# Optimization experiments

Hardware: AMD Instinct MI355X
Metric: run time of the kernel (lower is better)

Reference implementation:

```python
import jax, jax.numpy as jnp
import numpy as np

N_NODES = 100000
N_EDGES = 3200000
Q = 32
DT = 0.1
XI_MIN, XI_MAX = 0.0, 75.0


def setup_inputs() -> dict:
    key = jax.random.key(0)
    k1, k2, k3, k4, k5, k6 = jax.random.split(key, 6)
    f_distribution = jax.random.uniform(k1, (N_NODES, Q), dtype=jnp.float32)
    collision_term = jax.random.normal(k2, (N_NODES, Q), dtype=jnp.float32) * 0.01
    source_term = jax.random.normal(k3, (N_NODES, Q), dtype=jnp.float32) * 0.01
    edge_weight = jax.random.uniform(k4, (N_EDGES,), dtype=jnp.float32)
    src = jax.random.randint(k5, (N_EDGES,), 0, N_NODES, dtype=jnp.int32)
    dst = jax.random.randint(k6, (N_EDGES,), 0, N_NODES, dtype=jnp.int32)
    return {
        "f_distribution": f_distribution,
        "collision_term": collision_term,
        "source_term": source_term,
        "edge_weight": edge_weight,
        "src": src,
        "dst": dst,
    }


def _transport(f, edge_weight, src, dst):
    # xi velocity grid, one scalar per mesoscale channel q
    xi = jnp.linspace(XI_MIN, XI_MAX, Q, dtype=f.dtype)  # [Q]
    n = f.shape[0]
    # out-degree of each node in the (self-loop-free) graph
    out_deg = jax.ops.segment_sum(jnp.ones_like(edge_weight), src, num_segments=n)
    inv_out_deg = 1.0 / jnp.maximum(out_deg, 1.0)  # guard isolated nodes
    # per-edge message: (1/out_deg[src]) * xi * (f[dst]-f[src]) * w_e  -> [E, Q]
    f_diff = f[dst] - f[src]
    msg = (inv_out_deg[src] * edge_weight)[:, None] * xi[None, :] * f_diff
    # inflow: sum of messages at the destination node (original graph update_all)
    inflow = jax.ops.segment_sum(msg, dst, num_segments=n)
    # outflow: same per-edge quantity scattered back to the source node
    # (reverse-graph update_all with in_degree of reverse == out_degree of original)
    outflow = jax.ops.segment_sum(msg, src, num_segments=n)
    return outflow - inflow


def reference(f_distribution, collision_term, source_term, edge_weight, src, dst):
    f = jnp.maximum(f_distribution, 0.0)
    transport = _transport(f, edge_weight, src, dst)
    f_new = f - DT * (transport - collision_term - source_term)
    return jnp.maximum(f_new, 0.0)
```

## Files before the change

### kernel.cpp

```cpp
#include <hip/hip_runtime.h>
#include <hip/hip_fp16.h>

#define N_NODES 100000
#define N_EDGES 3200000
#define QCH 32
#define QP 16
#define DT_C 0.1f

#define NCHUNK 256
#define CHUNK_E (N_EDGES / NCHUNK)
#define HALF_NODES 50000
#define WORDS_HALF 12500
#define WORDS_TOT 25000

__global__ __launch_bounds__(256) void hist_kernel(const int* __restrict__ src,
                                                   unsigned int* __restrict__ part) {
    __shared__ unsigned int h[WORDS_HALF];
    int tid = threadIdx.x;
    int chunk = blockIdx.x >> 1;
    int rh = blockIdx.x & 1;
    int r0 = rh * HALF_NODES;
    for (int i = tid; i < WORDS_HALF; i += 256) h[i] = 0u;
    __syncthreads();
    int e0 = chunk * CHUNK_E;
    for (int e = e0 + tid; e < e0 + CHUNK_E; e += 256) {
        int n = src[e] - r0;
        if ((unsigned)n < HALF_NODES)
            atomicAdd(&h[n >> 2], 1u << (8 * (n & 3)));
    }
    __syncthreads();
    unsigned int* dstp = part + (size_t)chunk * WORDS_TOT + rh * WORDS_HALF;
    for (int i = tid; i < WORDS_HALF; i += 256) dstp[i] = h[i];
}

__global__ __launch_bounds__(256) void degsum_kernel(
        const unsigned int* __restrict__ part, float* __restrict__ deg) {
    int wd = blockIdx.x * 256 + threadIdx.x;
    if (wd >= WORDS_TOT) return;
    unsigned int s0 = 0, s1 = 0, s2 = 0, s3 = 0;
#pragma unroll 8
    for (int i = 0; i < NCHUNK; ++i) {
        unsigned int v = part[(size_t)i * WORDS_TOT + wd];
        s0 += v & 255u;
        s1 += (v >> 8) & 255u;
        s2 += (v >> 16) & 255u;
        s3 += v >> 24;
    }
    *(float4*)(deg + 4 * wd) =
        make_float4((float)s0, (float)s1, (float)s2, (float)s3);
}

__global__ void edge_kernel_h2(const float2* __restrict__ f2,
                               const float* __restrict__ w,
                               const int* __restrict__ src,
                               const int* __restrict__ dst,
                               const float* __restrict__ deg,
                               __half2* __restrict__ trans, int E) {
    long long t = (long long)blockIdx.x * blockDim.x + threadIdx.x;
    int e = (int)(t >> 4);
    int qp = (int)(t & 15);
    if (e >= E) return;
    int s = src[e];
    int d = dst[e];
    float coef = w[e] / fmaxf(deg[s], 1.0f);
    float2 fs = f2[s * QP + qp];
    float2 fd = f2[d * QP + qp];
    float xi0 = (75.0f / 31.0f) * (float)(2 * qp);
    float xi1 = (75.0f / 31.0f) * (float)(2 * qp + 1);
    float m0 = coef * xi0 * (fmaxf(fd.x, 0.0f) - fmaxf(fs.x, 0.0f));
    float m1 = coef * xi1 * (fmaxf(fd.y, 0.0f) - fmaxf(fs.y, 0.0f));
    unsafeAtomicAdd(&trans[s * QP + qp], __floats2half2_rn(m0, m1));
    unsafeAtomicAdd(&trans[d * QP + qp], __floats2half2_rn(-m0, -m1));
}

__global__ void final_f4(const float4* __restrict__ fdist,
                         const float4* __restrict__ coll,
                         const float4* __restrict__ srct,
                         const __half2* __restrict__ trans,
                         float4* __restrict__ out, int n4) {
    int i = blockIdx.x * blockDim.x + threadIdx.x;
    if (i >= n4) return;
    float2 t0 = __half22float2(trans[2 * i]);
    float2 t1 = __half22float2(trans[2 * i + 1]);
    float4 fr = fdist[i];
    float4 cl = coll[i];
    float4 st = srct[i];
    float4 o;
    o.x = fmaxf(fmaxf(fr.x, 0.0f) - DT_C * (t0.x - cl.x - st.x), 0.0f);
    o.y = fmaxf(fmaxf(fr.y, 0.0f) - DT_C * (t0.y - cl.y - st.y), 0.0f);
    o.z = fmaxf(fmaxf(fr.z, 0.0f) - DT_C * (t1.x - cl.z - st.z), 0.0f);
    o.w = fmaxf(fmaxf(fr.w, 0.0f) - DT_C * (t1.y - cl.w - st.w), 0.0f);
    out[i] = o;
}

__global__ void deg_kernel_f(const int* __restrict__ src,
                             float* __restrict__ deg, int E) {
    int e = blockIdx.x * blockDim.x + threadIdx.x;
    if (e < E) atomicAdd(&deg[src[e]], 1.0f);
}

extern "C" void kernel_launch(void* const* d_in, const int* in_sizes, int n_in,
                              void* d_out, int out_size, void* d_ws, size_t ws_size,
                              hipStream_t stream) {
    const float* f    = (const float*)d_in[0];
    const float* coll = (const float*)d_in[1];
    const float* srct = (const float*)d_in[2];
    const float* w    = (const float*)d_in[3];
    const int*   src  = (const int*)d_in[4];
    const int*   dst  = (const int*)d_in[5];
    float* out = (float*)d_out;

    const int N = N_NODES;
    const int E = N_EDGES;

    const size_t TRANS_B = (size_t)N * QP * sizeof(__half2);
    const size_t DEG_B   = (size_t)N * sizeof(float);
    const size_t PART_B  = (size_t)NCHUNK * WORDS_TOT * sizeof(unsigned int);

    __half2* trans = (__half2*)d_ws;
    float*   deg   = (float*)((char*)d_ws + TRANS_B);
    unsigned int* part = (unsigned int*)((char*)deg + DEG_B);

    hipMemsetAsync(trans, 0, TRANS_B, stream);

    if (ws_size >= TRANS_B + DEG_B + PART_B) {
        hist_kernel<<<2 * NCHUNK, 256, 0, stream>>>(src, part);
        degsum_kernel<<<(WORDS_TOT + 255) / 256, 256, 0, stream>>>(part, deg);
    } else {
        hipMemsetAsync(deg, 0, DEG_B, stream);
        deg_kernel_f<<<(E + 255) / 256, 256, 0, stream>>>(src, deg, E);
    }

    long long total = (long long)E * QP;
    int blocks = (int)((total + 255) / 256);
    edge_kernel_h2<<<blocks, 256, 0, stream>>>((const float2*)f, w, src, dst,
                                               deg, trans, E);

    int n4 = N * QCH / 4;
    final_f4<<<(n4 + 255) / 256, 256, 0, stream>>>((const float4*)f,
                                                   (const float4*)coll,
                                                   (const float4*)srct,
                                                   trans, (float4*)out, n4);
}
```

Before: 364.4 us.

## Fuse memset, degree sum, edge scatter and finalize into one cooperative kernel

Replaces the memset, degree-reduction, edge scatter and final update launches with a single cooperative persistent kernel that uses grid-wide syncs between phases. It also halves the number of histogram chunks to cut the cost of the partial-sum reduction. This removes launch overhead and the separate memset, at the cost of a grid-stride edge loop with fewer resident threads, which may hide atomic and gather latency less well. If the cooperative launch fails, the code falls back to the old multi-kernel path.

```diff
diff --git a/kernel.cpp b/kernel.cpp
--- a/kernel.cpp
+++ b/kernel.cpp
@@ -1,5 +1,8 @@
 #include <hip/hip_runtime.h>
 #include <hip/hip_fp16.h>
+#include <hip/hip_cooperative_groups.h>
+
+namespace cg = cooperative_groups;
 
 #define N_NODES 100000
 #define N_EDGES 3200000
@@ -7,11 +10,14 @@
 #define QP 16
 #define DT_C 0.1f
 
-#define NCHUNK 256
+#define NCHUNK 128
 #define CHUNK_E (N_EDGES / NCHUNK)
 #define HALF_NODES 50000
 #define WORDS_HALF 12500
 #define WORDS_TOT 25000
+
+#define COOP_BLOCKS 1024
+#define COOP_THREADS 256
 
 __global__ __launch_bounds__(256) void hist_kernel(const int* __restrict__ src,
                                                    unsigned int* __restrict__ part) {
@@ -32,6 +38,75 @@
     unsigned int* dstp = part + (size_t)chunk * WORDS_TOT + rh * WORDS_HALF;
     for (int i = tid; i < WORDS_HALF; i += 256) dstp[i] = h[i];
 }
+
+__global__ __launch_bounds__(COOP_THREADS, 4) void fused_kernel(
+        const float2* __restrict__ f2,
+        const float4* __restrict__ coll4,
+        const float4* __restrict__ srct4,
+        const float* __restrict__ w,
+        const int* __restrict__ src,
+        const int* __restrict__ dst,
+        const unsigned int* __restrict__ part,
+        float* __restrict__ deg,
+        __half2* __restrict__ trans,
+        float4* __restrict__ out) {
+    cg::grid_group grid = cg::this_grid();
+    int tid = blockIdx.x * blockDim.x + threadIdx.x;
+    int nthr = gridDim.x * blockDim.x;
+
+    float4* t4 = (float4*)trans;
+    for (int i = tid; i < (N_NODES * QCH) / 8; i += nthr)
+        t4[i] = make_float4(0.0f, 0.0f, 0.0f, 0.0f);
+    for (int wd = tid; wd < WORDS_TOT; wd += nthr) {
+        unsigned int s0 = 0, s1 = 0, s2 = 0, s3 = 0;
+#pragma unroll 8
+        for (int c = 0; c < NCHUNK; ++c) {
+            unsigned int v = part[(size_t)c * WORDS_TOT + wd];
+            s0 += v & 255u;
+            s1 += (v >> 8) & 255u;
+            s2 += (v >> 16) & 255u;
+            s3 += v >> 24;
+        }
+        *(float4*)(deg + 4 * wd) =
+            make_float4((float)s0, (float)s1, (float)s2, (float)s3);
+    }
+    grid.sync();
+
+    long long total = (long long)N_EDGES * QP;
+    for (long long t = tid; t < total; t += nthr) {
+        int e = (int)(t >> 4);
+        int qp = (int)(t & 15);
+        int s = src[e];
+        int d = dst[e];
+        float coef = w[e] / fmaxf(deg[s], 1.0f);
+        float2 fs = f2[s * QP + qp];
+        float2 fd = f2[d * QP + qp];
+        float xi0 = (75.0f / 31.0f) * (float)(2 * qp);
+        float xi1 = (75.0f / 31.0f) * (float)(2 * qp + 1);
+        float m0 = coef * xi0 * (fmaxf(fd.x, 0.0f) - fmaxf(fs.x, 0.0f));
+        float m1 = coef * xi1 * (fmaxf(fd.y, 0.0f) - fmaxf(fs.y, 0.0f));
+        unsafeAtomicAdd(&trans[s * QP + qp], __floats2half2_rn(m0, m1));
+        unsafeAtomicAdd(&trans[d * QP + qp], __floats2half2_rn(-m0, -m1));
+    }
+    grid.sync();
+
+    const float4* f4v = (const float4*)f2;
+    int n4 = N_NODES * QCH / 4;
+    for (int i = tid; i < n4; i += nthr) {
+        float2 t0 = __half22float2(trans[2 * i]);
+        float2 t1 = __half22float2(trans[2 * i + 1]);
+        float4 fr = f4v[i];
+        float4 cl = coll4[i];
+        float4 st = srct4[i];
+        float4 o;
+        o.x = fmaxf(fmaxf(fr.x, 0.0f) - DT_C * (t0.x - cl.x - st.x), 0.0f);
+        o.y = fmaxf(fmaxf(fr.y, 0.0f) - DT_C * (t0.y - cl.y - st.y), 0.0f);
+        o.z = fmaxf(fmaxf(fr.z, 0.0f) - DT_C * (t1.x - cl.z - st.z), 0.0f);
+        o.w = fmaxf(fmaxf(fr.w, 0.0f) - DT_C * (t1.y - cl.w - st.w), 0.0f);
+        out[i] = o;
+    }
+}
+
 
 __global__ __launch_bounds__(256) void degsum_kernel(
         const unsigned int* __restrict__ part, float* __restrict__ deg) {
@@ -99,6 +174,7 @@
     if (e < E) atomicAdd(&deg[src[e]], 1.0f);
 }
 
+
 extern "C" void kernel_launch(void* const* d_in, const int* in_sizes, int n_in,
                               void* d_out, int out_size, void* d_ws, size_t ws_size,
                               hipStream_t stream) {
@@ -121,12 +197,28 @@
     float*   deg   = (float*)((char*)d_ws + TRANS_B);
     unsigned int* part = (unsigned int*)((char*)deg + DEG_B);
 
-    hipMemsetAsync(trans, 0, TRANS_B, stream);
-
-    if (ws_size >= TRANS_B + DEG_B + PART_B) {
+    bool have_part = ws_size >= TRANS_B + DEG_B + PART_B;
+
+    if (have_part) {
         hist_kernel<<<2 * NCHUNK, 256, 0, stream>>>(src, part);
+
+        const float2* f2p   = (const float2*)f;
+        const float4* coll4 = (const float4*)coll;
+        const float4* srct4 = (const float4*)srct;
+        float4* out4 = (float4*)out;
+        void* args[] = {(void*)&f2p, (void*)&coll4, (void*)&srct4,
+                        (void*)&w, (void*)&src, (void*)&dst,
+                        (void*)&part, (void*)&deg, (void*)&trans,
+                        (void*)&out4};
+        hipError_t err = hipLaunchCooperativeKernel(
+            (const void*)fused_kernel, dim3(COOP_BLOCKS), dim3(COOP_THREADS),
+            args, 0, stream);
+        if (err == hipSuccess) return;
+
+        hipMemsetAsync(trans, 0, TRANS_B, stream);
         degsum_kernel<<<(WORDS_TOT + 255) / 256, 256, 0, stream>>>(part, deg);
     } else {
+        hipMemsetAsync(trans, 0, TRANS_B, stream);
         hipMemsetAsync(deg, 0, DEG_B, stream);
         deg_kernel_f<<<(E + 255) / 256, 256, 0, stream>>>(src, deg, E);
     }
```

After: 573.6 us. 1.57x slower.
